# Kernel optimization log

Hardware: AMD Instinct MI355X
Metric: run time of the kernel (lower is better)

Reference implementation:

```python
import jax, jax.numpy as jnp
import numpy as np

WINDOW_SIZE = 11
SIGMA = 1.5
C1 = 0.01 ** 2
C2 = 0.03 ** 2


def _gaussian_window(window_size, sigma, dtype):
    coords = jnp.arange(window_size, dtype=dtype) - window_size // 2
    g = jnp.exp(-coords ** 2 / (2 * sigma ** 2))
    g = g / g.sum()
    return g[:, None] * g[None, :]  # [k, k]


def _depthwise_conv(x, kernel2d):
    # x: [N, C, H, W]; kernel2d: [k, k]
    C = x.shape[1]
    k = kernel2d.shape[0]
    w = jnp.broadcast_to(kernel2d[None, None], (C, 1, k, k))  # OIHW, groups=C
    pad = k // 2
    return jax.lax.conv_general_dilated(
        x, w, window_strides=(1, 1), padding=[(pad, pad), (pad, pad)],
        dimension_numbers=('NCHW', 'OIHW', 'NCHW'), feature_group_count=C)


def setup_inputs() -> dict:
    key = jax.random.key(0)
    k1, k2 = jax.random.split(key)
    shape = (32, 3, 512, 512)
    pred = jax.random.uniform(k1, shape, dtype=jnp.float32)
    target = jax.random.uniform(k2, shape, dtype=jnp.float32)
    return {"pred": pred, "target": target}


def reference(pred, target):
    win = _gaussian_window(WINDOW_SIZE, SIGMA, pred.dtype)
    mu_p = _depthwise_conv(pred, win)
    mu_t = _depthwise_conv(target, win)
    mu_p_sq = mu_p ** 2
    mu_t_sq = mu_t ** 2
    mu_pt = mu_p * mu_t
    sigma_p_sq = _depthwise_conv(pred ** 2, win) - mu_p_sq
    sigma_t_sq = _depthwise_conv(target ** 2, win) - mu_t_sq
    sigma_pt = _depthwise_conv(pred * target, win) - mu_pt
    ssim = ((2 * mu_pt + C1) * (2 * sigma_pt + C2)) / (
        (mu_p_sq + mu_t_sq + C1) * (sigma_p_sq + sigma_t_sq + C2))
    return 1.0 - ssim.mean()
```

## Files before the change

### kernel.cpp

```cpp
#include <hip/hip_runtime.h>


#define IMG_H   512
#define IMG_W   512
#define TH      64
#define NCHUNK  7
#define LROW    160
#define RING    8
#define SSIM_C1 1e-4f
#define SSIM_C2 9e-4f

typedef float v2f __attribute__((ext_vector_type(2)));

__device__ constexpr float G[11] = {
    0.00102838f, 0.00759879f, 0.03600078f, 0.10936070f, 0.21300563f,
    0.26601180f,
    0.21300563f, 0.10936070f, 0.03600078f, 0.00759879f, 0.00102838f
};

__device__ __forceinline__ void gload16(const float* g, float* l) {
    __builtin_amdgcn_global_load_lds(
        (const __attribute__((address_space(1))) float*)g,
        (__attribute__((address_space(3))) float*)l, 16, 0, 0);
}

template<int PH>
__device__ __forceinline__ void phase(const float* __restrict__ pplw,
                                      const float* __restrict__ tplw,
                                      int r0, int j0, int lane4,
                                      float (*B)[LROW],
                                      int lane, bool lv,
                                      v2f (&acc01)[11], v2f (&acc23)[11],
                                      float (&accpt)[11], float& lsum) {
    const int j = j0 + PH;

    {
        const int rg  = r0 + j;
        const int rgc = min(max(rg, 0), IMG_H - 1);
        const int sI  = (j + 5) & (RING - 1);
        const float* ps = pplw + (size_t)rgc * IMG_W + lane4;
        const float* ts = tplw + (size_t)rgc * IMG_W + lane4;
        if (lv) {
            gload16(ps, &B[sI][0]);
            gload16(ts, &B[sI][80]);
        }
    }

    asm volatile("s_waitcnt vmcnt(10)" ::: "memory");

    const int rgj = r0 - 5 + j;
    if (rgj >= 0 && rgj < IMG_H) {
        const int sR = j & (RING - 1);
        const float* Lb = &B[sR][lane + 3];
        v2f h01 = {0.f, 0.f};
        v2f h23 = {0.f, 0.f};
        float hpt = 0.f;
        #pragma unroll
        for (int k = 0; k < 11; ++k) {
            const float w = G[k];
            const v2f wv = {w, w};
            v2f v;
            v.x = Lb[k];
            v.y = Lb[k + 80];
            h01 = __builtin_elementwise_fma(wv, v, h01);
            const v2f wab = wv * v;
            h23 = __builtin_elementwise_fma(wab, v, h23);
            hpt = fmaf(wab.x, v.y, hpt);
        }
#define SCAT(s) { constexpr int m = ((s) - PH + 21) % 11;                    \
                  constexpr float w = G[10 - m];                             \
                  const v2f wv = {w, w};                                     \
                  acc01[s] = __builtin_elementwise_fma(wv, h01, acc01[s]);   \
                  acc23[s] = __builtin_elementwise_fma(wv, h23, acc23[s]);   \
                  accpt[s] = fmaf(w, hpt, accpt[s]); }
        SCAT(0) SCAT(1) SCAT(2) SCAT(3) SCAT(4) SCAT(5)
        SCAT(6) SCAT(7) SCAT(8) SCAT(9) SCAT(10)
#undef SCAT
    }

    constexpr int SE = (PH + 1) % 11;
    const int l = j - 10;
    if (l >= 0 && l < TH) {
        const float mp = acc01[SE].x, mt = acc01[SE].y;
        const float mpp = mp * mp, mtt = mt * mt, mpt = mp * mt;
        const float sp  = acc23[SE].x - mpp;
        const float st  = acc23[SE].y - mtt;
        const float spt = accpt[SE]   - mpt;
        const float num = (2.f * mpt + SSIM_C1) * (2.f * spt + SSIM_C2);
        const float den = (mpp + mtt + SSIM_C1) * (sp + st + SSIM_C2);
        lsum += num * __builtin_amdgcn_rcpf(den);
    }
    acc01[SE] = (v2f){0.f, 0.f};
    acc23[SE] = (v2f){0.f, 0.f};
    accpt[SE] = 0.f;
}

__global__ __launch_bounds__(256, 4) void ssim_main(const float* __restrict__ pred,
                                                    const float* __restrict__ targ,
                                                    float* __restrict__ ws) {
    __shared__ float B[4][RING][LROW];
    __shared__ float wsum[4];

    const int tid  = threadIdx.x;
    const int lane = tid & 63;
    const int wid  = tid >> 6;

    const int gt    = __builtin_amdgcn_readfirstlane(blockIdx.x * 4 + wid);
    const int c0    = (gt & 7) * TH;
    const int r0    = ((gt >> 3) & 7) * TH;
    const int plane = gt >> 6;
    const float* pplw = pred + (size_t)plane * (IMG_H * IMG_W) + (c0 - 8);
    const float* tplw = targ + (size_t)plane * (IMG_H * IMG_W) + (c0 - 8);

    float (*W)[LROW] = B[wid];

    const int  lane4 = lane * 4;
    const int  gc0   = c0 - 8 + lane4;
    const bool lv    = (lane < 20) && (gc0 >= 0) && (gc0 <= IMG_W - 4);

    if (lane < 20 && !lv) {
        #pragma unroll
        for (int s = 0; s < RING; ++s) {
            #pragma unroll
            for (int w = 0; w < 4; ++w) {
                W[s][lane4 + w]      = 0.f;
                W[s][80 + lane4 + w] = 0.f;
            }
        }
    }

    #pragma unroll
    for (int r = 0; r < 5; ++r) {
        const int rg  = max(r0 - 5 + r, 0);
        const float* ps = pplw + (size_t)rg * IMG_W + lane4;
        const float* ts = tplw + (size_t)rg * IMG_W + lane4;
        if (lv) {
            gload16(ps, &W[r][0]);
            gload16(ts, &W[r][80]);
        }
    }

    v2f   acc01[11];
    v2f   acc23[11];
    float accpt[11];
    #pragma unroll
    for (int s = 0; s < 11; ++s) {
        acc01[s] = (v2f){0.f, 0.f};
        acc23[s] = (v2f){0.f, 0.f};
        accpt[s] = 0.f;
    }

    float lsum = 0.f;

    for (int chunk = 0; chunk < NCHUNK; ++chunk) {
        const int j0 = chunk * 11;
#define P(n) phase<n>(pplw, tplw, r0, j0, lane4, W, lane, lv, \
                      acc01, acc23, accpt, lsum);
        P(0) P(1) P(2) P(3) P(4) P(5) P(6) P(7) P(8) P(9) P(10)
#undef P
    }

    #pragma unroll
    for (int off = 32; off > 0; off >>= 1) lsum += __shfl_down(lsum, off);
    if (lane == 0) wsum[wid] = lsum;
    __syncthreads();
    if (tid == 0) ws[blockIdx.x] = wsum[0] + wsum[1] + wsum[2] + wsum[3];
}

__global__ __launch_bounds__(256) void ssim_finalize(const float* __restrict__ ws,
                                                     float* __restrict__ out) {
    __shared__ float wsum[4];
    const int tid  = threadIdx.x;
    const int lane = tid & 63;
    const int wid  = tid >> 6;
    float s = 0.f;
    #pragma unroll
    for (int i = 0; i < 6; ++i) s += ws[tid + 256 * i];
    #pragma unroll
    for (int off = 32; off > 0; off >>= 1) s += __shfl_down(s, off);
    if (lane == 0) wsum[wid] = s;
    __syncthreads();
    if (tid == 0) {
        const float tot = wsum[0] + wsum[1] + wsum[2] + wsum[3];
        out[0] = 1.0f - tot * (1.0f / 25165824.0f);
    }
}

extern "C" void kernel_launch(void* const* d_in, const int* in_sizes, int n_in,
                              void* d_out, int out_size, void* d_ws, size_t ws_size,
                              hipStream_t stream) {
    (void)in_sizes; (void)n_in; (void)out_size; (void)ws_size;
    const float* pred = (const float*)d_in[0];
    const float* targ = (const float*)d_in[1];
    float* ws  = (float*)d_ws;
    float* out = (float*)d_out;

    ssim_main<<<dim3(1536), 256, 0, stream>>>(pred, targ, ws);
    ssim_finalize<<<1, 256, 0, stream>>>(ws, out);
}
```

Measured before the change: 253.6 us.

## Software-pipeline LDS row reads into register double buffer one row ahead

Each phase now reads the next row's 11-tap window from LDS into a register double buffer while it computes the horizontal pass on the current row, which was loaded the phase before. Global prefetch moves one row further ahead, and the prologue fills six ring rows. The loop is unrolled by pairs of chunks so buffer parity stays compile-time. The aim is to hide LDS read latency behind FMA work, at the cost of about 44 extra VGPRs, which may lower occupancy under launch_bounds(256,4) and risks ring slot reuse hazards with only an 8-row ring.

```diff
diff --git a/kernel.cpp b/kernel.cpp
--- a/kernel.cpp
+++ b/kernel.cpp
@@ -4,7 +4,6 @@
 #define IMG_H   512
 #define IMG_W   512
 #define TH      64
-#define NCHUNK  7
 #define LROW    160
 #define RING    8
 #define SSIM_C1 1e-4f
@@ -24,20 +23,23 @@
         (__attribute__((address_space(3))) float*)l, 16, 0, 0);
 }
 
-template<int PH>
+template<int PH, int PAR>
 __device__ __forceinline__ void phase(const float* __restrict__ pplw,
                                       const float* __restrict__ tplw,
                                       int r0, int j0, int lane4,
                                       float (*B)[LROW],
                                       int lane, bool lv,
+                                      v2f (&vbuf)[2][11],
                                       v2f (&acc01)[11], v2f (&acc23)[11],
                                       float (&accpt)[11], float& lsum) {
     const int j = j0 + PH;
+    constexpr int CUR = (PH + PAR) & 1;
+    constexpr int NXT = CUR ^ 1;
 
     {
-        const int rg  = r0 + j;
+        const int rg  = r0 + j + 1;
         const int rgc = min(max(rg, 0), IMG_H - 1);
-        const int sI  = (j + 5) & (RING - 1);
+        const int sI  = (j + 6) & (RING - 1);
         const float* ps = pplw + (size_t)rgc * IMG_W + lane4;
         const float* ts = tplw + (size_t)rgc * IMG_W + lane4;
         if (lv) {
@@ -48,10 +50,26 @@
 
     asm volatile("s_waitcnt vmcnt(10)" ::: "memory");
 
+    {
+        const int rg1 = r0 - 4 + j;
+        if (rg1 >= 0 && rg1 < IMG_H) {
+            const int sR1 = (j + 1) & (RING - 1);
+            const float* Lb = &B[sR1][lane + 3];
+            #pragma unroll
+            for (int k = 0; k < 11; ++k) {
+                v2f v;
+                v.x = Lb[k];
+                v.y = Lb[k + 80];
+                vbuf[NXT][k] = v;
+            }
+        } else {
+            #pragma unroll
+            for (int k = 0; k < 11; ++k) vbuf[NXT][k] = (v2f){0.f, 0.f};
+        }
+    }
+
     const int rgj = r0 - 5 + j;
     if (rgj >= 0 && rgj < IMG_H) {
-        const int sR = j & (RING - 1);
-        const float* Lb = &B[sR][lane + 3];
         v2f h01 = {0.f, 0.f};
         v2f h23 = {0.f, 0.f};
         float hpt = 0.f;
@@ -59,9 +77,7 @@
         for (int k = 0; k < 11; ++k) {
             const float w = G[k];
             const v2f wv = {w, w};
-            v2f v;
-            v.x = Lb[k];
-            v.y = Lb[k + 80];
+            const v2f v = vbuf[CUR][k];
             h01 = __builtin_elementwise_fma(wv, v, h01);
             const v2f wab = wv * v;
             h23 = __builtin_elementwise_fma(wab, v, h23);
@@ -130,7 +146,7 @@
     }
 
     #pragma unroll
-    for (int r = 0; r < 5; ++r) {
+    for (int r = 0; r < 6; ++r) {
         const int rg  = max(r0 - 5 + r, 0);
         const float* ps = pplw + (size_t)rg * IMG_W + lane4;
         const float* ts = tplw + (size_t)rg * IMG_W + lane4;
@@ -140,6 +156,7 @@
         }
     }
 
+    v2f   vbuf[2][11];
     v2f   acc01[11];
     v2f   acc23[11];
     float accpt[11];
@@ -150,15 +167,40 @@
         accpt[s] = 0.f;
     }
 
+    asm volatile("s_waitcnt vmcnt(10)" ::: "memory");
+    {
+        if (r0 - 5 >= 0) {
+            const float* Lb = &W[0][lane + 3];
+            #pragma unroll
+            for (int k = 0; k < 11; ++k) {
+                v2f v;
+                v.x = Lb[k];
+                v.y = Lb[k + 80];
+                vbuf[0][k] = v;
+            }
+        } else {
+            #pragma unroll
+            for (int k = 0; k < 11; ++k) vbuf[0][k] = (v2f){0.f, 0.f};
+        }
+    }
+
     float lsum = 0.f;
 
-    for (int chunk = 0; chunk < NCHUNK; ++chunk) {
-        const int j0 = chunk * 11;
-#define P(n) phase<n>(pplw, tplw, r0, j0, lane4, W, lane, lv, \
-                      acc01, acc23, accpt, lsum);
-        P(0) P(1) P(2) P(3) P(4) P(5) P(6) P(7) P(8) P(9) P(10)
+#define P(n, PAR) phase<n, PAR>(pplw, tplw, r0, j0, lane4, W, lane, lv, \
+                                vbuf, acc01, acc23, accpt, lsum);
+#define CHNK(PAR) { P(0,PAR) P(1,PAR) P(2,PAR) P(3,PAR) P(4,PAR) P(5,PAR) \
+                    P(6,PAR) P(7,PAR) P(8,PAR) P(9,PAR) P(10,PAR) }
+
+    int j0 = 0;
+    for (int c = 0; c < 3; ++c) {
+        CHNK(0)
+        j0 += 11;
+        CHNK(1)
+        j0 += 11;
+    }
+    CHNK(0)
+#undef CHNK
 #undef P
-    }
 
     #pragma unroll
     for (int off = 32; off > 0; off >>= 1) lsum += __shfl_down(lsum, off);
```

Result: slower. 818.6 us (+222.8%).

## Software-pipeline horizontal pass one row ahead of vertical scatter

Applied to the files above, without the earlier changes.

Computes the horizontal Gaussian pass for row j+1 while scattering row j's already-computed results into the vertical accumulators. The results are held in two ping-pong register structs, with chunk parity unrolled so their roles swap at compile time. The goal is to hide LDS read latency behind the FMA-heavy scatter. The prefetch ring now runs one row further ahead, with 6 rows preloaded. The row-validity branch becomes a multiply-by-mask, which removes divergent control flow but always does the work, raises register pressure, and leaves a tighter prefetch distance inside the 8-slot ring.

```diff
diff --git a/kernel.cpp b/kernel.cpp
--- a/kernel.cpp
+++ b/kernel.cpp
@@ -4,13 +4,14 @@
 #define IMG_H   512
 #define IMG_W   512
 #define TH      64
-#define NCHUNK  7
 #define LROW    160
 #define RING    8
 #define SSIM_C1 1e-4f
 #define SSIM_C2 9e-4f
 
 typedef float v2f __attribute__((ext_vector_type(2)));
+
+struct Hp { v2f h01; v2f h23; float hpt; };
 
 __device__ constexpr float G[11] = {
     0.00102838f, 0.00759879f, 0.03600078f, 0.10936070f, 0.21300563f,
@@ -25,19 +26,20 @@
 }
 
 template<int PH>
-__device__ __forceinline__ void phase(const float* __restrict__ pplw,
-                                      const float* __restrict__ tplw,
-                                      int r0, int j0, int lane4,
-                                      float (*B)[LROW],
-                                      int lane, bool lv,
-                                      v2f (&acc01)[11], v2f (&acc23)[11],
-                                      float (&accpt)[11], float& lsum) {
+__device__ __forceinline__ void phase_body(const float* __restrict__ pplw,
+                                           const float* __restrict__ tplw,
+                                           int r0, int j0, int lane4,
+                                           float (*B)[LROW],
+                                           int lane, bool lv,
+                                           Hp& cur, Hp& nxt,
+                                           v2f (&acc01)[11], v2f (&acc23)[11],
+                                           float (&accpt)[11], float& lsum) {
     const int j = j0 + PH;
 
     {
-        const int rg  = r0 + j;
+        const int rg  = r0 + j + 1;
         const int rgc = min(max(rg, 0), IMG_H - 1);
-        const int sI  = (j + 5) & (RING - 1);
+        const int sI  = (j + 6) & (RING - 1);
         const float* ps = pplw + (size_t)rgc * IMG_W + lane4;
         const float* ts = tplw + (size_t)rgc * IMG_W + lane4;
         if (lv) {
@@ -48,35 +50,37 @@
 
     asm volatile("s_waitcnt vmcnt(10)" ::: "memory");
 
-    const int rgj = r0 - 5 + j;
-    if (rgj >= 0 && rgj < IMG_H) {
-        const int sR = j & (RING - 1);
+    {
+        const int sR = (j + 1) & (RING - 1);
         const float* Lb = &B[sR][lane + 3];
         v2f h01 = {0.f, 0.f};
         v2f h23 = {0.f, 0.f};
         float hpt = 0.f;
-        #pragma unroll
-        for (int k = 0; k < 11; ++k) {
-            const float w = G[k];
-            const v2f wv = {w, w};
-            v2f v;
-            v.x = Lb[k];
-            v.y = Lb[k + 80];
-            h01 = __builtin_elementwise_fma(wv, v, h01);
-            const v2f wab = wv * v;
-            h23 = __builtin_elementwise_fma(wab, v, h23);
-            hpt = fmaf(wab.x, v.y, hpt);
-        }
+#define CV(i) { const v2f wv = {G[i], G[i]};                                 \
+                v2f v; v.x = Lb[i]; v.y = Lb[i + 80];                        \
+                h01 = __builtin_elementwise_fma(wv, v, h01);                 \
+                const v2f wab = wv * v;                                      \
+                h23 = __builtin_elementwise_fma(wab, v, h23);                \
+                hpt = fmaf(wab.x, v.y, hpt); }
+        CV(0) CV(1) CV(2) CV(3) CV(4) CV(5) CV(6) CV(7) CV(8) CV(9) CV(10)
+#undef CV
+        const int grow = r0 - 4 + j;
+        const float m  = (grow >= 0 && grow < IMG_H) ? 1.f : 0.f;
+        const v2f mv = {m, m};
+        nxt.h01 = h01 * mv;
+        nxt.h23 = h23 * mv;
+        nxt.hpt = hpt * m;
+    }
+
 #define SCAT(s) { constexpr int m = ((s) - PH + 21) % 11;                    \
                   constexpr float w = G[10 - m];                             \
                   const v2f wv = {w, w};                                     \
-                  acc01[s] = __builtin_elementwise_fma(wv, h01, acc01[s]);   \
-                  acc23[s] = __builtin_elementwise_fma(wv, h23, acc23[s]);   \
-                  accpt[s] = fmaf(w, hpt, accpt[s]); }
-        SCAT(0) SCAT(1) SCAT(2) SCAT(3) SCAT(4) SCAT(5)
-        SCAT(6) SCAT(7) SCAT(8) SCAT(9) SCAT(10)
+                  acc01[s] = __builtin_elementwise_fma(wv, cur.h01, acc01[s]); \
+                  acc23[s] = __builtin_elementwise_fma(wv, cur.h23, acc23[s]); \
+                  accpt[s] = fmaf(w, cur.hpt, accpt[s]); }
+    SCAT(0) SCAT(1) SCAT(2) SCAT(3) SCAT(4) SCAT(5)
+    SCAT(6) SCAT(7) SCAT(8) SCAT(9) SCAT(10)
 #undef SCAT
-    }
 
     constexpr int SE = (PH + 1) % 11;
     const int l = j - 10;
@@ -95,6 +99,23 @@
     accpt[SE] = 0.f;
 }
 
+template<int PH, int PAR>
+__device__ __forceinline__ void phase(const float* __restrict__ pplw,
+                                      const float* __restrict__ tplw,
+                                      int r0, int j0, int lane4,
+                                      float (*B)[LROW],
+                                      int lane, bool lv,
+                                      Hp& HA, Hp& HB,
+                                      v2f (&acc01)[11], v2f (&acc23)[11],
+                                      float (&accpt)[11], float& lsum) {
+    if constexpr (((PH + PAR) & 1) == 0)
+        phase_body<PH>(pplw, tplw, r0, j0, lane4, B, lane, lv,
+                       HA, HB, acc01, acc23, accpt, lsum);
+    else
+        phase_body<PH>(pplw, tplw, r0, j0, lane4, B, lane, lv,
+                       HB, HA, acc01, acc23, accpt, lsum);
+}
+
 __global__ __launch_bounds__(256, 4) void ssim_main(const float* __restrict__ pred,
                                                     const float* __restrict__ targ,
                                                     float* __restrict__ ws) {
@@ -130,7 +151,7 @@
     }
 
     #pragma unroll
-    for (int r = 0; r < 5; ++r) {
+    for (int r = 0; r < 6; ++r) {
         const int rg  = max(r0 - 5 + r, 0);
         const float* ps = pplw + (size_t)rg * IMG_W + lane4;
         const float* ts = tplw + (size_t)rg * IMG_W + lane4;
@@ -150,15 +171,48 @@
         accpt[s] = 0.f;
     }
 
+    Hp HA, HB;
+    HA.h01 = (v2f){0.f, 0.f}; HA.h23 = (v2f){0.f, 0.f}; HA.hpt = 0.f;
+    HB.h01 = (v2f){0.f, 0.f}; HB.h23 = (v2f){0.f, 0.f}; HB.hpt = 0.f;
+
+    asm volatile("s_waitcnt vmcnt(10)" ::: "memory");
+    {
+        const float* Lb = &W[0][lane + 3];
+        v2f h01 = {0.f, 0.f};
+        v2f h23 = {0.f, 0.f};
+        float hpt = 0.f;
+#define CV(i) { const v2f wv = {G[i], G[i]};                                 \
+                v2f v; v.x = Lb[i]; v.y = Lb[i + 80];                        \
+                h01 = __builtin_elementwise_fma(wv, v, h01);                 \
+                const v2f wab = wv * v;                                      \
+                h23 = __builtin_elementwise_fma(wab, v, h23);                \
+                hpt = fmaf(wab.x, v.y, hpt); }
+        CV(0) CV(1) CV(2) CV(3) CV(4) CV(5) CV(6) CV(7) CV(8) CV(9) CV(10)
+#undef CV
+        const float m = (r0 - 5 >= 0) ? 1.f : 0.f;
+        const v2f mv = {m, m};
+        HA.h01 = h01 * mv;
+        HA.h23 = h23 * mv;
+        HA.hpt = hpt * m;
+    }
+
     float lsum = 0.f;
 
-    for (int chunk = 0; chunk < NCHUNK; ++chunk) {
-        const int j0 = chunk * 11;
-#define P(n) phase<n>(pplw, tplw, r0, j0, lane4, W, lane, lv, \
-                      acc01, acc23, accpt, lsum);
-        P(0) P(1) P(2) P(3) P(4) P(5) P(6) P(7) P(8) P(9) P(10)
+#define P(n, PAR) phase<n, PAR>(pplw, tplw, r0, j0, lane4, W, lane, lv, \
+                                HA, HB, acc01, acc23, accpt, lsum);
+#define CHNK(PAR) { P(0,PAR) P(1,PAR) P(2,PAR) P(3,PAR) P(4,PAR) P(5,PAR) \
+                    P(6,PAR) P(7,PAR) P(8,PAR) P(9,PAR) P(10,PAR) }
+
+    int j0 = 0;
+    for (int c = 0; c < 3; ++c) {
+        CHNK(0)
+        j0 += 11;
+        CHNK(1)
+        j0 += 11;
+    }
+    CHNK(0)
+#undef CHNK
 #undef P
-    }
 
     #pragma unroll
     for (int off = 32; off > 0; off >>= 1) lsum += __shfl_down(lsum, off);
```

Measured after the change: 867.2 us. 3.42x slower.
